# Optimization experiments

Measured on AMD Instinct MI355X. Metric: run time of the kernel, lower is better.

The kernel has to match this reference:

```python
import jax, jax.numpy as jnp
import numpy as np

B = 8; H = 128; W = 128; C = 256
NH = 16; HD = 16          # head_dim hard-coded to 16 in source
WS = 8; SS = 4            # window size / shift size
HID = 1024                # mlp hidden = 4 * C
SCALE = HD ** (-0.5)


def _rel_pos_index(ws):
    # same construction as torch buffer relative_position_index
    coords = np.stack(np.meshgrid(np.arange(ws), np.arange(ws), indexing='ij')).reshape(2, -1)
    rel = (coords[:, :, None] - coords[:, None, :]).transpose(1, 2, 0).copy()
    rel[..., 0] += ws - 1
    rel[..., 1] += ws - 1
    rel[..., 0] *= 2 * ws - 1
    return rel.sum(-1)  # (N, N) ints


def _attn_mask(h, w, ws, ss):
    # shifted-window mask, matches calculate_mask()
    img = np.zeros((h, w))
    sl = (slice(0, -ws), slice(-ws, -ss), slice(-ss, None))
    c = 0
    for hs in sl:
        for wsl in sl:
            img[hs, wsl] = c
            c += 1
    mw = img.reshape(h // ws, ws, w // ws, ws).transpose(0, 2, 1, 3).reshape(-1, ws * ws)
    d = mw[:, None, :] - mw[:, :, None]  # (nW, N, N)
    return np.where(d == 0, 0.0, -100.0).astype(np.float32)


def _ln(x, g, b, eps=1e-5):
    m = x.mean(-1, keepdims=True)
    v = ((x - m) ** 2).mean(-1, keepdims=True)
    return (x - m) * jax.lax.rsqrt(v + eps) * g + b


def setup_inputs() -> dict:
    key = jax.random.key(0)
    ks = jax.random.split(key, 12)
    inner = NH * HD
    std = 0.02
    return {
        'x': jax.random.normal(ks[0], (B, H * W, C), jnp.float32),
        'ln1_g': jnp.ones((C,), jnp.float32),
        'ln1_b': jnp.zeros((C,), jnp.float32),
        'q_w': jax.random.normal(ks[1], (C, inner), jnp.float32) * std,
        'q_b': jnp.zeros((inner,), jnp.float32),
        'k_w': jax.random.normal(ks[2], (C, inner), jnp.float32) * std,
        'k_b': jnp.zeros((inner,), jnp.float32),
        'v_w': jax.random.normal(ks[3], (C, inner), jnp.float32) * std,
        'v_b': jnp.zeros((inner,), jnp.float32),
        'rpb': jax.random.normal(ks[4], ((2 * WS - 1) * (2 * WS - 1), NH), jnp.float32) * std,
        'proj_w': jax.random.normal(ks[5], (inner, C), jnp.float32) * std,
        'proj_b': jnp.zeros((C,), jnp.float32),
        'ln2_g': jnp.ones((C,), jnp.float32),
        'ln2_b': jnp.zeros((C,), jnp.float32),
        'fc1_w': jax.random.normal(ks[6], (C, HID), jnp.float32) * std,
        'fc1_b': jnp.zeros((HID,), jnp.float32),
        'fc2_w': jax.random.normal(ks[7], (HID, C), jnp.float32) * std,
        'fc2_b': jnp.zeros((C,), jnp.float32),
        'H_in': 128,
        'W_in': 128,
    }


def reference(x, ln1_g, ln1_b, q_w, q_b, k_w, k_b, v_w, v_b, rpb,
              proj_w, proj_b, ln2_g, ln2_b, fc1_w, fc1_b, fc2_w, fc2_b,
              H_in, W_in):
    N = WS * WS
    nW = (H // WS) * (W // WS)
    idx = _rel_pos_index(WS)                       # static int (N, N)
    mask = jnp.asarray(_attn_mask(H, W, WS, SS))   # (nW, N, N)

    shortcut = x
    h = _ln(x, ln1_g, ln1_b).reshape(B, H, W, C)
    h = jnp.roll(h, (-SS, -SS), axis=(1, 2))
    # window partition -> (B*nW, N, C)
    h = h.reshape(B, H // WS, WS, W // WS, WS, C).transpose(0, 1, 3, 2, 4, 5)
    h = h.reshape(B * nW, N, C)

    q = (h @ q_w + q_b).reshape(-1, N, NH, HD).transpose(0, 2, 1, 3) * SCALE
    k = (h @ k_w + k_b).reshape(-1, N, NH, HD).transpose(0, 2, 1, 3)
    v = (h @ v_w + v_b).reshape(-1, N, NH, HD).transpose(0, 2, 1, 3)

    attn = jnp.einsum('bhnd,bhmd->bhnm', q, k)     # (B*nW, NH, N, N)
    bias = rpb[idx.reshape(-1)].reshape(N, N, NH).transpose(2, 0, 1)
    attn = attn + bias[None]
    attn = attn.reshape(B, nW, NH, N, N) + mask[None, :, None]
    attn = jax.nn.softmax(attn.reshape(B * nW, NH, N, N), axis=-1)

    o = jnp.einsum('bhnm,bhmd->bhnd', attn, v)
    o = o.transpose(0, 2, 1, 3).reshape(B * nW, N, NH * HD)
    o = o @ proj_w + proj_b

    # window reverse + roll back
    o = o.reshape(B, H // WS, W // WS, WS, WS, C).transpose(0, 1, 3, 2, 4, 5)
    o = o.reshape(B, H, W, C)
    o = jnp.roll(o, (SS, SS), axis=(1, 2)).reshape(B, H * W, C)

    x = shortcut + o
    h2 = _ln(x, ln2_g, ln2_b)
    h2 = jax.nn.gelu(h2 @ fc1_w + fc1_b, approximate=False)
    return x + (h2 @ fc2_w + fc2_b)
```

## Files before the change

kernel.cpp:

```cpp
#include <hip/hip_runtime.h>
#include <hip/hip_bf16.h>
#include <stdint.h>


#define SLOT ((size_t)64 << 20)

typedef __attribute__((ext_vector_type(8))) short bf16x8;
typedef __attribute__((ext_vector_type(4))) float f32x4;

union FU { float f; unsigned u; };

__device__ inline float bflo(unsigned p) { FU x; x.u = p << 16; return x.f; }
__device__ inline float bfhi(unsigned p) { FU x; x.u = p & 0xffff0000u; return x.f; }
__device__ inline unsigned short f2bf(float f) {
  FU x; x.f = f;
  unsigned r = x.u + 0x7fff + ((x.u >> 16) & 1);
  return (unsigned short)(r >> 16);
}
__device__ inline unsigned packbf2(float a, float b) {
  FU x, y; x.f = a; y.f = b;
  unsigned ra = (x.u + 0x7fff + ((x.u >> 16) & 1)) >> 16;
  unsigned rb = (y.u + 0x7fff + ((y.u >> 16) & 1)) & 0xffff0000u;
  return ra | rb;
}

__device__ inline float fast_gelu(float v) {
  return v / (1.0f + __expf(-1.702f * v));
}

__device__ inline void gload16(const void* g, void* l) {
  __builtin_amdgcn_global_load_lds(
      (const __attribute__((address_space(1))) unsigned int*)g,
      (__attribute__((address_space(3))) unsigned int*)l, 16, 0, 0);
}


__global__ __launch_bounds__(256) void build_qkvw(
    const float* __restrict__ qw, const float* __restrict__ kw, const float* __restrict__ vw,
    const float* __restrict__ qb, const float* __restrict__ kb, const float* __restrict__ vb,
    unsigned short* __restrict__ wt, float* __restrict__ bias) {
  int i = blockIdx.x * 256 + threadIdx.x;
  if (i < 768 * 256) {
    int n = i >> 8, c = i & 255;
    const float* w = (n < 256) ? qw : (n < 512 ? kw : vw);
    const float sc = (n < 256) ? 0.25f : 1.0f;
    int nn = n & 255;
    wt[i] = f2bf(sc * w[c * 256 + nn]);
  }
  if (i < 768) {
    bias[i] = (i < 256) ? 0.25f * qb[i] : (i < 512 ? kb[i - 256] : vb[i - 512]);
  }
}

__global__ __launch_bounds__(256) void wconv_t(
    const float* __restrict__ src, unsigned short* __restrict__ dst, int R, int C) {
  int i = blockIdx.x * 256 + threadIdx.x;
  if (i >= R * C) return;
  int n = i / R, c = i - n * R;
  dst[i] = f2bf(src[(size_t)c * C + n]);
}

__global__ __launch_bounds__(256) void ln1_roll_win(
    const float* __restrict__ x, const float* __restrict__ g, const float* __restrict__ b,
    unsigned short* __restrict__ hwin) {
  const int tok = blockIdx.x * 4 + (threadIdx.x >> 6);
  const int l = threadIdx.x & 63;
  const int n = tok & 63, wi = (tok >> 6) & 255, bb = tok >> 14;
  const int wh = wi >> 4, ww = wi & 15, r = n >> 3, c = n & 7;
  const int hs = (wh * 8 + r + 4) & 127;
  const int wsx = (ww * 8 + c + 4) & 127;
  const float* xr = x + ((size_t)bb * 16384 + hs * 128 + wsx) * 256;
  float4 v = *(const float4*)(xr + l * 4);
  float s = v.x + v.y + v.z + v.w;
#pragma unroll
  for (int off = 32; off; off >>= 1) s += __shfl_xor(s, off);
  const float mean = s * (1.f / 256.f);
  const float d0 = v.x - mean, d1 = v.y - mean, d2 = v.z - mean, d3 = v.w - mean;
  float vv = d0 * d0 + d1 * d1 + d2 * d2 + d3 * d3;
#pragma unroll
  for (int off = 32; off; off >>= 1) vv += __shfl_xor(vv, off);
  const float rs = rsqrtf(vv * (1.f / 256.f) + 1e-5f);
  float4 gg = *(const float4*)(g + l * 4);
  float4 bv = *(const float4*)(b + l * 4);
  uint2 outv;
  outv.x = packbf2(d0 * rs * gg.x + bv.x, d1 * rs * gg.y + bv.y);
  outv.y = packbf2(d2 * rs * gg.z + bv.z, d3 * rs * gg.w + bv.w);
  *(uint2*)(hwin + (size_t)tok * 256 + l * 4) = outv;
}

template <int EPI, int K, int N, int NBX>
__global__ __launch_bounds__(256) void gemm128(
    const unsigned short* __restrict__ A, const unsigned short* __restrict__ Bt,
    const float* __restrict__ bias, unsigned short* __restrict__ Cb,
    float* __restrict__ Cf) {
  __shared__ __align__(16) unsigned short smem[2][2][128 * 64];
  const int nwg = gridDim.x;
  const int q = nwg >> 3;
  const int swz = (blockIdx.x & 7) * q + (blockIdx.x >> 3);
  const int m0 = (swz / NBX) * 128;
  const int n0 = (swz % NBX) * 128;

  const int t = threadIdx.x, w = t >> 6, l = t & 63;
  const int lg = l >> 4, lm = l & 15;
  const int wr = w >> 1, wc = w & 1;

  const int srow = w * 32 + (l >> 3);
  const int scol = ((l & 7) ^ (l >> 3)) * 8;
  const unsigned short* Ap = A + (size_t)(m0 + srow) * K + scol;
  const unsigned short* Bp = Bt + (size_t)(n0 + srow) * K + scol;

  const int cb = n0 + wc * 64 + lm;
  f32x4 acc[4][4];
#pragma unroll
  for (int n = 0; n < 4; ++n) {
    const float bv = bias[cb + n * 16];
#pragma unroll
    for (int m = 0; m < 4; ++m) acc[m][n] = (f32x4){bv, bv, bv, bv};
  }

  constexpr int NT = K >> 6;
  const int cx = lg ^ (lm & 7);

#pragma unroll
  for (int i = 0; i < 4; ++i) {
    gload16(Ap + (size_t)(i * 8) * K, &smem[0][0][(w * 32 + i * 8) * 64]);
    gload16(Bp + (size_t)(i * 8) * K, &smem[0][1][(w * 32 + i * 8) * 64]);
  }
  __syncthreads();

#pragma unroll
  for (int kt = 0; kt < NT; ++kt) {
    const int cur = kt & 1;
    if (kt + 1 < NT) {
      const int ko = (kt + 1) << 6;
#pragma unroll
      for (int i = 0; i < 4; ++i) {
        gload16(Ap + (size_t)(i * 8) * K + ko, &smem[cur ^ 1][0][(w * 32 + i * 8) * 64]);
        gload16(Bp + (size_t)(i * 8) * K + ko, &smem[cur ^ 1][1][(w * 32 + i * 8) * 64]);
      }
    }
#pragma unroll
    for (int kk = 0; kk < 64; kk += 32) {
      const int ch = (cx ^ (kk >> 3)) * 8;
      bf16x8 af[4], bfr[4];
#pragma unroll
      for (int m = 0; m < 4; ++m)
        af[m] = *(const bf16x8*)&smem[cur][0][(wr * 64 + m * 16 + lm) * 64 + ch];
#pragma unroll
      for (int n = 0; n < 4; ++n)
        bfr[n] = *(const bf16x8*)&smem[cur][1][(wc * 64 + n * 16 + lm) * 64 + ch];
#pragma unroll
      for (int m = 0; m < 4; ++m)
#pragma unroll
        for (int n = 0; n < 4; ++n)
          acc[m][n] = __builtin_amdgcn_mfma_f32_16x16x32_bf16(af[m], bfr[n], acc[m][n], 0, 0, 0);
    }
    if (kt + 1 < NT) __syncthreads();
  }

  __syncthreads();
  float* Lp = (float*)smem;
#pragma unroll
  for (int m = 0; m < 4; ++m) {
#pragma unroll
    for (int n = 0; n < 4; ++n) {
      const int col = wc * 64 + n * 16 + lm;
#pragma unroll
      for (int r = 0; r < 4; ++r) {
        const int row = wr * 64 + m * 16 + lg * 4 + r;
        Lp[row * 128 + (col ^ (lg << 4))] = acc[m][n][r];
      }
    }
  }
  __syncthreads();
  const int rr0 = w * 32 + (l >> 5);
  const int cg = (l & 31) * 4;
#pragma unroll
  for (int p = 0; p < 16; ++p) {
    const int row = rr0 + p * 2;
    const int sc = cg ^ (((row >> 2) & 3) << 4);
    float4 v = *(const float4*)&Lp[row * 128 + sc];
    if (EPI == 2) {
      v.x = fast_gelu(v.x); v.y = fast_gelu(v.y);
      v.z = fast_gelu(v.z); v.w = fast_gelu(v.w);
    }
    if (EPI == 3) {
      float4* op = (float4*)&Cf[(size_t)(m0 + row) * N + n0 + cg];
      float4 o = *op;
      o.x += v.x; o.y += v.y; o.z += v.z; o.w += v.w;
      *op = o;
    } else {
      uint2 pk;
      pk.x = packbf2(v.x, v.y);
      pk.y = packbf2(v.z, v.w);
      *(uint2*)&Cb[(size_t)(m0 + row) * N + n0 + cg] = pk;
    }
  }
}

__global__ __launch_bounds__(256) void attn_mfma(
    const unsigned short* __restrict__ qkv, const float* __restrict__ rpb,
    unsigned short* __restrict__ o) {
  __shared__ float rps[16][226];
  __shared__ __align__(16) unsigned short Pl[4][64][72];
  const int win = blockIdx.x;
  const int wh = (win >> 4) & 15, ww = win & 15;
  const int t = threadIdx.x, wv = t >> 6, l = t & 63;
  const int lg = l >> 4, lm = l & 15;
  const unsigned short* base = qkv + (size_t)win * 64 * 768;

  for (int i = t; i < 3600; i += 256) rps[i & 15][i >> 4] = rpb[i];
  __syncthreads();

  const bool eH = (wh == 15), eW = (ww == 15);
  const bool edge = eH || eW;

  int qv[4], liq[4];
#pragma unroll
  for (int nt = 0; nt < 4; ++nt) {
    const int qn = nt * 16 + lm, ri = qn >> 3, ci = qn & 7;
    qv[nt] = ri * 15 + ci;
    liq[nt] = (eH ? (ri < 4 ? 1 : 2) : 0) * 3 + (eW ? (ci < 4 ? 1 : 2) : 0);
  }
  int kv[4][4], ljk[4][4];
#pragma unroll
  for (int mt = 0; mt < 4; ++mt)
#pragma unroll
    for (int r = 0; r < 4; ++r) {
      const int kn = mt * 16 + 4 * lg + r, rj = kn >> 3, cj = kn & 7;
      kv[mt][r] = rj * 15 + cj;
      ljk[mt][r] = (eH ? (rj < 4 ? 1 : 2) : 0) * 3 + (eW ? (cj < 4 ? 1 : 2) : 0);
    }

  const bf16x8 zf = {0, 0, 0, 0, 0, 0, 0, 0};

#pragma unroll 1
  for (int hi = 0; hi < 4; ++hi) {
    const int h = wv * 4 + hi;
    bf16x8 kf[4], qf[4];
#pragma unroll
    for (int i = 0; i < 4; ++i) {
      kf[i] = (lg < 2)
          ? *(const bf16x8*)(base + (size_t)(i * 16 + lm) * 768 + 256 + h * 16 + lg * 8)
          : zf;
      qf[i] = (lg < 2)
          ? *(const bf16x8*)(base + (size_t)(i * 16 + lm) * 768 + h * 16 + lg * 8)
          : zf;
    }
    f32x4 acc[4][4];
#pragma unroll
    for (int mt = 0; mt < 4; ++mt)
#pragma unroll
      for (int nt = 0; nt < 4; ++nt)
        acc[mt][nt] = (f32x4){0.f, 0.f, 0.f, 0.f};
#pragma unroll
    for (int mt = 0; mt < 4; ++mt)
#pragma unroll
      for (int nt = 0; nt < 4; ++nt)
        acc[mt][nt] = __builtin_amdgcn_mfma_f32_16x16x32_bf16(kf[mt], qf[nt], acc[mt][nt], 0, 0, 0);

#pragma unroll
    for (int nt = 0; nt < 4; ++nt) {
      float mx = -1e30f;
#pragma unroll
      for (int mt = 0; mt < 4; ++mt)
#pragma unroll
        for (int r = 0; r < 4; ++r) {
          float s = acc[mt][nt][r] + rps[h][qv[nt] - kv[mt][r] + 112];
          if (edge) s += (liq[nt] == ljk[mt][r]) ? 0.f : -100.f;
          acc[mt][nt][r] = s;
          mx = fmaxf(mx, s);
        }
      mx = fmaxf(mx, __shfl_xor(mx, 16));
      mx = fmaxf(mx, __shfl_xor(mx, 32));
      float sum = 0.f;
#pragma unroll
      for (int mt = 0; mt < 4; ++mt)
#pragma unroll
        for (int r = 0; r < 4; ++r) {
          const float p = __expf(acc[mt][nt][r] - mx);
          acc[mt][nt][r] = p;
          sum += p;
        }
      sum += __shfl_xor(sum, 16);
      sum += __shfl_xor(sum, 32);
      const float inv = 1.f / sum;
      const int qn = nt * 16 + lm;
#pragma unroll
      for (int mt = 0; mt < 4; ++mt) {
        uint2 pk;
        pk.x = packbf2(acc[mt][nt][0] * inv, acc[mt][nt][1] * inv);
        pk.y = packbf2(acc[mt][nt][2] * inv, acc[mt][nt][3] * inv);
        *(uint2*)&Pl[wv][qn][mt * 16 + 4 * lg] = pk;
      }
    }

    f32x4 oacc[4];
#pragma unroll
    for (int mt = 0; mt < 4; ++mt) oacc[mt] = (f32x4){0.f, 0.f, 0.f, 0.f};
#pragma unroll
    for (int kk = 0; kk < 2; ++kk) {
      bf16x8 vf;
#pragma unroll
      for (int j = 0; j < 8; ++j)
        vf[j] = (short)base[(size_t)(kk * 32 + lg * 8 + j) * 768 + 512 + h * 16 + lm];
#pragma unroll
      for (int mt = 0; mt < 4; ++mt) {
        bf16x8 pf = *(const bf16x8*)&Pl[wv][mt * 16 + lm][kk * 32 + lg * 8];
        oacc[mt] = __builtin_amdgcn_mfma_f32_16x16x32_bf16(pf, vf, oacc[mt], 0, 0, 0);
      }
    }
#pragma unroll
    for (int mt = 0; mt < 4; ++mt)
#pragma unroll
      for (int r = 0; r < 4; ++r)
        o[((size_t)win * 64 + mt * 16 + 4 * lg + r) * 256 + h * 16 + lm] = f2bf(oacc[mt][r]);
  }
}

__global__ __launch_bounds__(256) void scatter_ln2(
    const float* __restrict__ x, const unsigned short* __restrict__ po,
    const float* __restrict__ g, const float* __restrict__ b,
    float* __restrict__ x2, unsigned short* __restrict__ h2) {
  const int tok = blockIdx.x * 4 + (threadIdx.x >> 6);
  const int l = threadIdx.x & 63;
  const int bb = tok >> 14, pix = tok & 16383, hy = pix >> 7, wx = pix & 127;
  const int hr = (hy + 124) & 127, wc = (wx + 124) & 127;
  const int src = ((bb << 8) + (hr >> 3) * 16 + (wc >> 3)) * 64 + (hr & 7) * 8 + (wc & 7);
  float4 xv = *(const float4*)(x + (size_t)tok * 256 + l * 4);
  uint2 pv = *(const uint2*)(po + (size_t)src * 256 + l * 4);
  const float y0 = xv.x + bflo(pv.x);
  const float y1 = xv.y + bfhi(pv.x);
  const float y2 = xv.z + bflo(pv.y);
  const float y3 = xv.w + bfhi(pv.y);
  *(float4*)(x2 + (size_t)tok * 256 + l * 4) = make_float4(y0, y1, y2, y3);
  float s = y0 + y1 + y2 + y3;
#pragma unroll
  for (int off = 32; off; off >>= 1) s += __shfl_xor(s, off);
  const float mean = s * (1.f / 256.f);
  const float d0 = y0 - mean, d1 = y1 - mean, d2 = y2 - mean, d3 = y3 - mean;
  float vv = d0 * d0 + d1 * d1 + d2 * d2 + d3 * d3;
#pragma unroll
  for (int off = 32; off; off >>= 1) vv += __shfl_xor(vv, off);
  const float rs = rsqrtf(vv * (1.f / 256.f) + 1e-5f);
  float4 gg = *(const float4*)(g + l * 4);
  float4 bv = *(const float4*)(b + l * 4);
  uint2 outv;
  outv.x = packbf2(d0 * rs * gg.x + bv.x, d1 * rs * gg.y + bv.y);
  outv.y = packbf2(d2 * rs * gg.z + bv.z, d3 * rs * gg.w + bv.w);
  *(uint2*)(h2 + (size_t)tok * 256 + l * 4) = outv;
}


extern "C" void kernel_launch(void* const* d_in, const int* in_sizes, int n_in,
                              void* d_out, int out_size, void* d_ws, size_t ws_size,
                              hipStream_t stream) {
  const float* x = (const float*)d_in[0];
  const float* ln1g = (const float*)d_in[1];
  const float* ln1b = (const float*)d_in[2];
  const float* qw = (const float*)d_in[3];
  const float* qb = (const float*)d_in[4];
  const float* kw = (const float*)d_in[5];
  const float* kb = (const float*)d_in[6];
  const float* vw = (const float*)d_in[7];
  const float* vb = (const float*)d_in[8];
  const float* rpb = (const float*)d_in[9];
  const float* pw = (const float*)d_in[10];
  const float* pb = (const float*)d_in[11];
  const float* ln2g = (const float*)d_in[12];
  const float* ln2b = (const float*)d_in[13];
  const float* f1w = (const float*)d_in[14];
  const float* f1b = (const float*)d_in[15];
  const float* f2w = (const float*)d_in[16];
  const float* f2b = (const float*)d_in[17];
  float* out = (float*)d_out;

  char* wsb = (char*)d_ws;
  unsigned short* hwin = (unsigned short*)(wsb);
  unsigned short* qkv = (unsigned short*)(wsb + SLOT);
  unsigned short* po = (unsigned short*)(wsb + 4 * SLOT);
  unsigned short* g1 = qkv;
  unsigned short* wqkvt = (unsigned short*)(wsb + 5 * SLOT);
  unsigned short* projt = wqkvt + 768 * 256;
  unsigned short* fc1t = projt + 256 * 256;
  unsigned short* fc2t = fc1t + 1024 * 256;
  float* bqkv = (float*)(fc2t + 256 * 1024);

  build_qkvw<<<768, 256, 0, stream>>>(qw, kw, vw, qb, kb, vb, wqkvt, bqkv);
  wconv_t<<<256, 256, 0, stream>>>(pw, projt, 256, 256);
  wconv_t<<<1024, 256, 0, stream>>>(f1w, fc1t, 256, 1024);
  wconv_t<<<1024, 256, 0, stream>>>(f2w, fc2t, 1024, 256);

  ln1_roll_win<<<32768, 256, 0, stream>>>(x, ln1g, ln1b, hwin);
  gemm128<0, 256, 768, 6><<<6 * 1024, 256, 0, stream>>>(hwin, wqkvt, bqkv, qkv, nullptr);
  attn_mfma<<<2048, 256, 0, stream>>>(qkv, rpb, hwin);
  gemm128<0, 256, 256, 2><<<2 * 1024, 256, 0, stream>>>(hwin, projt, pb, po, nullptr);
  scatter_ln2<<<32768, 256, 0, stream>>>(x, po, ln2g, ln2b, out, hwin);
  gemm128<2, 256, 1024, 8><<<8 * 1024, 256, 0, stream>>>(hwin, fc1t, f1b, g1, nullptr);
  gemm128<3, 1024, 256, 2><<<2 * 1024, 256, 0, stream>>>(g1, fc2t, f2b, nullptr, out);
}
```

Measured before the change: 688.1 us.

## Fuse output projection GEMM with window-reverse, residual add and LayerNorm2

Replaces the separate projection GEMM and scatter_ln2 kernels with one kernel. Each 512-thread block computes a 256-row by 256-column projection tile with MFMA, stages the fp32 result through swizzled LDS, then applies the inverse shift/window scatter, residual add and LayerNorm in-place. This removes the bf16 round trip of the projection output through global memory and one launch, and also keeps the projection result in fp32 before the residual. In exchange it uses large LDS and register footprints with only 512 blocks, which may limit occupancy.

```diff
diff --git a/kernel.cpp b/kernel.cpp
--- a/kernel.cpp
+++ b/kernel.cpp
@@ -198,6 +198,125 @@
   }
 }
 
+__global__ __launch_bounds__(512, 2) void proj_ln2(
+    const unsigned short* __restrict__ A, const unsigned short* __restrict__ Bt,
+    const float* __restrict__ bias, const float* __restrict__ x,
+    const float* __restrict__ g2, const float* __restrict__ b2,
+    float* __restrict__ out, unsigned short* __restrict__ h2) {
+  constexpr int K = 256;
+  __shared__ __align__(16) unsigned short smem[2][2][256 * 64];
+  const int nwg = gridDim.x;
+  const int q = nwg >> 3;
+  const int swz = (blockIdx.x & 7) * q + (blockIdx.x >> 3);
+  const int m0 = swz * 256;
+
+  const int t = threadIdx.x, w = t >> 6, l = t & 63;
+  const int lg = l >> 4, lm = l & 15;
+  const int wr = w >> 2, wn = w & 3;
+
+  const int srow = w * 8 + (l >> 3);
+  const int scol = ((l & 7) ^ (l >> 3)) * 8;
+  const unsigned short* Ap = A + (size_t)(m0 + srow) * K + scol;
+  const unsigned short* Bp = Bt + (size_t)srow * K + scol;
+
+  f32x4 acc[8][4];
+#pragma unroll
+  for (int n = 0; n < 4; ++n) {
+    const float bv = bias[wn * 64 + n * 16 + lm];
+#pragma unroll
+    for (int m = 0; m < 8; ++m) acc[m][n] = (f32x4){bv, bv, bv, bv};
+  }
+
+  const int cx = lg ^ (lm & 7);
+
+#pragma unroll
+  for (int i = 0; i < 4; ++i) {
+    gload16(Ap + (size_t)(i * 64) * K, &smem[0][0][(i * 64 + w * 8) * 64]);
+    gload16(Bp + (size_t)(i * 64) * K, &smem[0][1][(i * 64 + w * 8) * 64]);
+  }
+  __syncthreads();
+
+#pragma unroll
+  for (int kt = 0; kt < 4; ++kt) {
+    const int cur = kt & 1;
+    if (kt + 1 < 4) {
+      const int ko = (kt + 1) << 6;
+#pragma unroll
+      for (int i = 0; i < 4; ++i) {
+        gload16(Ap + (size_t)(i * 64) * K + ko, &smem[cur ^ 1][0][(i * 64 + w * 8) * 64]);
+        gload16(Bp + (size_t)(i * 64) * K + ko, &smem[cur ^ 1][1][(i * 64 + w * 8) * 64]);
+      }
+    }
+#pragma unroll
+    for (int kk = 0; kk < 64; kk += 32) {
+      const int ch = (cx ^ (kk >> 3)) * 8;
+      bf16x8 af[8], bfr[4];
+#pragma unroll
+      for (int m = 0; m < 8; ++m)
+        af[m] = *(const bf16x8*)&smem[cur][0][(wr * 128 + m * 16 + lm) * 64 + ch];
+#pragma unroll
+      for (int n = 0; n < 4; ++n)
+        bfr[n] = *(const bf16x8*)&smem[cur][1][(wn * 64 + n * 16 + lm) * 64 + ch];
+#pragma unroll
+      for (int m = 0; m < 8; ++m)
+#pragma unroll
+        for (int n = 0; n < 4; ++n)
+          acc[m][n] = __builtin_amdgcn_mfma_f32_16x16x32_bf16(af[m], bfr[n], acc[m][n], 0, 0, 0);
+    }
+    if (kt + 1 < 4) __syncthreads();
+  }
+
+  float* Lf = (float*)smem;
+  const float4 g4 = *(const float4*)(g2 + l * 4);
+  const float4 bb4 = *(const float4*)(b2 + l * 4);
+#pragma unroll
+  for (int h = 0; h < 2; ++h) {
+    __syncthreads();
+    if (wr == h) {
+#pragma unroll
+      for (int m = 0; m < 8; ++m)
+#pragma unroll
+        for (int n = 0; n < 4; ++n) {
+          const int col = wn * 64 + n * 16 + lm;
+#pragma unroll
+          for (int r = 0; r < 4; ++r) {
+            const int rowl = m * 16 + lg * 4 + r;
+            Lf[rowl * 256 + (col ^ (lg << 4))] = acc[m][n][r];
+          }
+        }
+    }
+    __syncthreads();
+#pragma unroll
+    for (int it = 0; it < 16; ++it) {
+      const int rowl = it * 8 + w;
+      const int sc = (l * 4) ^ (((rowl >> 2) & 3) << 4);
+      float4 v = *(const float4*)&Lf[rowl * 256 + sc];
+      const int src = m0 + h * 128 + rowl;
+      const int bb = src >> 14, wi = (src >> 6) & 255, n = src & 63;
+      const int hy = ((wi >> 4) * 8 + (n >> 3) + 4) & 127;
+      const int wx = ((wi & 15) * 8 + (n & 7) + 4) & 127;
+      const size_t dst = ((size_t)(bb << 14) + hy * 128 + wx) * 256;
+      float4 xv = *(const float4*)(x + dst + l * 4);
+      const float y0 = xv.x + v.x, y1 = xv.y + v.y;
+      const float y2 = xv.z + v.z, y3 = xv.w + v.w;
+      *(float4*)(out + dst + l * 4) = make_float4(y0, y1, y2, y3);
+      float s = y0 + y1 + y2 + y3;
+#pragma unroll
+      for (int off = 32; off; off >>= 1) s += __shfl_xor(s, off);
+      const float mean = s * (1.f / 256.f);
+      const float d0 = y0 - mean, d1 = y1 - mean, d2 = y2 - mean, d3 = y3 - mean;
+      float vv = d0 * d0 + d1 * d1 + d2 * d2 + d3 * d3;
+#pragma unroll
+      for (int off = 32; off; off >>= 1) vv += __shfl_xor(vv, off);
+      const float rs = rsqrtf(vv * (1.f / 256.f) + 1e-5f);
+      uint2 outv;
+      outv.x = packbf2(d0 * rs * g4.x + bb4.x, d1 * rs * g4.y + bb4.y);
+      outv.y = packbf2(d2 * rs * g4.z + bb4.z, d3 * rs * g4.w + bb4.w);
+      *(uint2*)(h2 + dst + l * 4) = outv;
+    }
+  }
+}
+
 __global__ __launch_bounds__(256) void attn_mfma(
     const unsigned short* __restrict__ qkv, const float* __restrict__ rpb,
     unsigned short* __restrict__ o) {
@@ -316,39 +435,6 @@
       for (int r = 0; r < 4; ++r)
         o[((size_t)win * 64 + mt * 16 + 4 * lg + r) * 256 + h * 16 + lm] = f2bf(oacc[mt][r]);
   }
-}
-
-__global__ __launch_bounds__(256) void scatter_ln2(
-    const float* __restrict__ x, const unsigned short* __restrict__ po,
-    const float* __restrict__ g, const float* __restrict__ b,
-    float* __restrict__ x2, unsigned short* __restrict__ h2) {
-  const int tok = blockIdx.x * 4 + (threadIdx.x >> 6);
-  const int l = threadIdx.x & 63;
-  const int bb = tok >> 14, pix = tok & 16383, hy = pix >> 7, wx = pix & 127;
-  const int hr = (hy + 124) & 127, wc = (wx + 124) & 127;
-  const int src = ((bb << 8) + (hr >> 3) * 16 + (wc >> 3)) * 64 + (hr & 7) * 8 + (wc & 7);
-  float4 xv = *(const float4*)(x + (size_t)tok * 256 + l * 4);
-  uint2 pv = *(const uint2*)(po + (size_t)src * 256 + l * 4);
-  const float y0 = xv.x + bflo(pv.x);
-  const float y1 = xv.y + bfhi(pv.x);
-  const float y2 = xv.z + bflo(pv.y);
-  const float y3 = xv.w + bfhi(pv.y);
-  *(float4*)(x2 + (size_t)tok * 256 + l * 4) = make_float4(y0, y1, y2, y3);
-  float s = y0 + y1 + y2 + y3;
-#pragma unroll
-  for (int off = 32; off; off >>= 1) s += __shfl_xor(s, off);
-  const float mean = s * (1.f / 256.f);
-  const float d0 = y0 - mean, d1 = y1 - mean, d2 = y2 - mean, d3 = y3 - mean;
-  float vv = d0 * d0 + d1 * d1 + d2 * d2 + d3 * d3;
-#pragma unroll
-  for (int off = 32; off; off >>= 1) vv += __shfl_xor(vv, off);
-  const float rs = rsqrtf(vv * (1.f / 256.f) + 1e-5f);
-  float4 gg = *(const float4*)(g + l * 4);
-  float4 bv = *(const float4*)(b + l * 4);
-  uint2 outv;
-  outv.x = packbf2(d0 * rs * gg.x + bv.x, d1 * rs * gg.y + bv.y);
-  outv.y = packbf2(d2 * rs * gg.z + bv.z, d3 * rs * gg.w + bv.w);
-  *(uint2*)(h2 + (size_t)tok * 256 + l * 4) = outv;
 }
 
 
@@ -378,7 +464,7 @@
   char* wsb = (char*)d_ws;
   unsigned short* hwin = (unsigned short*)(wsb);
   unsigned short* qkv = (unsigned short*)(wsb + SLOT);
-  unsigned short* po = (unsigned short*)(wsb + 4 * SLOT);
+  unsigned short* ovec = (unsigned short*)(wsb + 4 * SLOT);
   unsigned short* g1 = qkv;
   unsigned short* wqkvt = (unsigned short*)(wsb + 5 * SLOT);
   unsigned short* projt = wqkvt + 768 * 256;
@@ -393,9 +479,8 @@
 
   ln1_roll_win<<<32768, 256, 0, stream>>>(x, ln1g, ln1b, hwin);
   gemm128<0, 256, 768, 6><<<6 * 1024, 256, 0, stream>>>(hwin, wqkvt, bqkv, qkv, nullptr);
-  attn_mfma<<<2048, 256, 0, stream>>>(qkv, rpb, hwin);
-  gemm128<0, 256, 256, 2><<<2 * 1024, 256, 0, stream>>>(hwin, projt, pb, po, nullptr);
-  scatter_ln2<<<32768, 256, 0, stream>>>(x, po, ln2g, ln2b, out, hwin);
+  attn_mfma<<<2048, 256, 0, stream>>>(qkv, rpb, ovec);
+  proj_ln2<<<512, 512, 0, stream>>>(ovec, projt, pb, x, ln2g, ln2b, out, hwin);
   gemm128<2, 256, 1024, 8><<<8 * 1024, 256, 0, stream>>>(hwin, fc1t, f1b, g1, nullptr);
   gemm128<3, 1024, 256, 2><<<2 * 1024, 256, 0, stream>>>(g1, fc2t, f2b, nullptr, out);
 }
```

Measured after the change: 685.7 us. No clear change (-0.4%).
